# Kernel tuning notes

Hardware: AMD Instinct MI355X
Metric: run time of the kernel (lower is better)

## Reference

```python
import jax, jax.numpy as jnp
import numpy as np

BINS = 5
POINTS = 2
EPS_DIV = 1e-6
GN_GROUPS = 32
GN_EPS = 1e-5


def bilinear_sum(img, ys, xs):
    """Sum of bilinear samples with zero padding outside the image.
    img: (B, C, H, W); ys, xs: (B, K, H, W) absolute sample coords.
    Returns (B, C, H, W) = sum over K of bilinear(img, ys_k, xs_k)."""
    B, C, H, W = img.shape
    K = ys.shape[1]
    y0 = jnp.floor(ys)
    x0 = jnp.floor(xs)
    imgf = img.reshape(B, C, H * W)
    acc = jnp.zeros((B, C, K, H, W), img.dtype)
    for dy, dx in ((0, 0), (0, 1), (1, 0), (1, 1)):
        yi = y0 + dy
        xi = x0 + dx
        w = (1.0 - jnp.abs(ys - yi)) * (1.0 - jnp.abs(xs - xi))
        valid = (yi >= 0) & (yi <= H - 1) & (xi >= 0) & (xi <= W - 1)
        yc = jnp.clip(yi, 0, H - 1).astype(jnp.int32)
        xc = jnp.clip(xi, 0, W - 1).astype(jnp.int32)
        idx = (yc * W + xc).reshape(B, 1, K * H * W)
        g = jnp.take_along_axis(imgf, idx, axis=2).reshape(B, C, K, H, W)
        acc = acc + (w * valid.astype(img.dtype))[:, None] * g
    return acc.sum(axis=2)


def setup_inputs():
    key = jax.random.key(0)
    ks = jax.random.split(key, 6)
    B, C, H, W = 2, 256, 100, 152
    P, K = POINTS, BINS
    x = jax.random.normal(ks[0], (B, C, H, W), jnp.float32)
    offsets = jax.random.normal(ks[1], (B, P * K * 2, H, W), jnp.float32) * 2.0
    ef_w = jax.random.normal(ks[2], (P * C, C), jnp.float32) * 0.02
    ef_b = jnp.zeros((P * C,), jnp.float32)
    hm1_w = jax.random.normal(ks[3], (P, C, C), jnp.float32) * 0.02
    hm1_b = jnp.zeros((P, C), jnp.float32)
    hm2_w = jax.random.normal(ks[4], (P, C), jnp.float32) * 0.02
    hm2_b = jnp.zeros((P,), jnp.float32)
    merge_w = jax.random.normal(ks[5], (C, P * C), jnp.float32) * 0.02
    merge_b = jnp.zeros((C,), jnp.float32)
    gn_g = jnp.ones((C,), jnp.float32)
    gn_b = jnp.zeros((C,), jnp.float32)
    return {"x": x, "offsets": offsets, "ef_w": ef_w, "ef_b": ef_b,
            "hm1_w": hm1_w, "hm1_b": hm1_b, "hm2_w": hm2_w, "hm2_b": hm2_b,
            "merge_w": merge_w, "merge_b": merge_b, "gn_g": gn_g, "gn_b": gn_b}


def reference(x, offsets, ef_w, ef_b, hm1_w, hm1_b, hm2_w, hm2_b, merge_w, merge_b, gn_g, gn_b):
    B, C, H, W = x.shape
    P, K = POINTS, BINS
    # expand_feat: 1x1 conv C -> P*C
    ef = jnp.einsum('bchw,dc->bdhw', x, ef_w) + ef_b[None, :, None, None]
    efp = ef.reshape(B, P, C, H, W)
    # heatmap: grouped 1x1 conv (per-point) -> ReLU -> grouped 1x1 conv -> exp
    h = jax.nn.relu(jnp.einsum('bpchw,pdc->bpdhw', efp, hm1_w) + hm1_b[None, :, :, None, None])
    heat = jnp.exp(jnp.einsum('bpdhw,pd->bphw', h, hm2_w) + hm2_b[None, :, None, None])  # (B,P,H,W)
    # offsets: (B, P, K, 2, H, W) with channel layout [y, x] per bin.
    # base_offset cancels the [1,bins] kernel grid, so the deform conv with
    # all-ones weights is simply: sum over bins of bilinear samples at
    # (h + off_y, w + off_x).
    off = offsets.reshape(B, P, K, 2, H, W)
    hg = jnp.arange(H, dtype=x.dtype)[None, None, None, :, None]
    wg = jnp.arange(W, dtype=x.dtype)[None, None, None, None, :]
    ys = hg + off[:, :, :, 0]  # (B,P,K,H,W)
    xs = wg + off[:, :, :, 1]
    outs = []
    for p in range(P):
        # sample feat*heat (C channels) and heat (1 channel) together
        img = jnp.concatenate([efp[:, p] * heat[:, p][:, None], heat[:, p][:, None]], axis=1)
        s = bilinear_sum(img, ys[:, p], xs[:, p])  # (B, C+1, H, W)
        outs.append(s[:, :C] / (s[:, C:] + EPS_DIV))
    outs = jnp.concatenate(outs, axis=1)  # (B, P*C, H, W)
    merged = jnp.einsum('bchw,dc->bdhw', outs, merge_w) + merge_b[None, :, None, None]
    # GroupNorm(32, C) + ReLU
    g = merged.reshape(B, GN_GROUPS, C // GN_GROUPS, H, W)
    mu = g.mean(axis=(2, 3, 4), keepdims=True)
    var = g.var(axis=(2, 3, 4), keepdims=True)
    gn = ((g - mu) / jnp.sqrt(var + GN_EPS)).reshape(B, C, H, W)
    gn = gn * gn_g[None, :, None, None] + gn_b[None, :, None, None]
    return jax.nn.relu(gn)
```

## Files before the change

### kernel.cpp

```cpp
#include <hip/hip_runtime.h>

#define BINS 5
#define PTS  2
constexpr int Bx = 2, Cc = 256, Hh = 100, Ww = 152;
constexpr int HW = Hh * Ww;
constexpr int NTILE = 238;
constexpr float EPS_DIV = 1e-6f;
constexpr float GN_EPS  = 1e-5f;

typedef __attribute__((ext_vector_type(8))) short bfrag;
typedef __attribute__((ext_vector_type(4))) float f32x4;

__device__ __forceinline__ ushort f2bf(float f) {
    union { float f; unsigned u; } v; v.f = f;
    unsigned r = v.u + 0x7fffu + ((v.u >> 16) & 1u);
    return (ushort)(r >> 16);
}
__device__ __forceinline__ float bflo(unsigned u) {
    return __uint_as_float(u << 16);
}
__device__ __forceinline__ float bfhi(unsigned u) {
    return __uint_as_float(u & 0xffff0000u);
}
__device__ __forceinline__ unsigned pack2(float a, float b) {
    return (unsigned)f2bf(a) | ((unsigned)f2bf(b) << 16);
}

__global__ __launch_bounds__(256)
void k_wconv(const float* __restrict__ efw, const float* __restrict__ w1,
             const float* __restrict__ mw, ushort* __restrict__ wb)
{
    int gid = blockIdx.x * 256 + threadIdx.x;
    int e = gid * 4;
    int arr = e >> 17, off = e & 131071;
    const float* src = arr == 0 ? efw : (arr == 1 ? w1 : mw);
    float4 v = *(const float4*)(src + off);
    ushort4 o = { f2bf(v.x), f2bf(v.y), f2bf(v.z), f2bf(v.w) };
    *(ushort4*)(wb + e) = o;
}

__global__ __launch_bounds__(256)
void k_ef(const float* __restrict__ x, const ushort* __restrict__ wbe,
          const float* __restrict__ efb, ushort* __restrict__ efp)
{
    __shared__ ushort As[128 * 72];
    __shared__ ushort Bs[64 * 72];
    const int t = threadIdx.x;
    const int wv = t >> 6, ln = t & 63;
    const int quad = ln >> 4, l16 = ln & 15;
    const int pix0 = blockIdx.x * 64;
    const int n0 = blockIdx.y * 128;
    const int b = blockIdx.z;
    const float* xb = x + (size_t)b * Cc * HW;

    f32x4 acc[2][4];
    #pragma unroll
    for (int i = 0; i < 2; i++)
        #pragma unroll
        for (int j = 0; j < 4; j++) acc[i][j] = (f32x4){0.f, 0.f, 0.f, 0.f};

    const int arow = t >> 3, acol = (t & 7) * 8;
    const int bpix = t & 63, bkg = (t >> 6) * 8;
    int pp = pix0 + bpix; if (pp > HW - 1) pp = HW - 1;

    for (int k0 = 0; k0 < 256; k0 += 64) {
        #pragma unroll
        for (int r = 0; r < 4; r++) {
            int row = arow + r * 32;
            *(uint4*)&As[row * 72 + acol] =
                *(const uint4*)&wbe[(size_t)(n0 + row) * 256 + k0 + acol];
        }
        #pragma unroll
        for (int r = 0; r < 2; r++) {
            int kc = bkg + r * 32;
            union { ushort s[8]; uint4 v; } tmp;
            #pragma unroll
            for (int j = 0; j < 8; j++)
                tmp.s[j] = f2bf(xb[(size_t)(k0 + kc + j) * HW + pp]);
            *(uint4*)&Bs[bpix * 72 + kc] = tmp.v;
        }
        __syncthreads();
        #pragma unroll
        for (int kk = 0; kk < 64; kk += 32) {
            bfrag af[2], bfr[4];
            #pragma unroll
            for (int dt = 0; dt < 2; dt++)
                af[dt] = *(const bfrag*)&As[(wv * 32 + dt * 16 + l16) * 72 + kk + quad * 8];
            #pragma unroll
            for (int pt = 0; pt < 4; pt++)
                bfr[pt] = *(const bfrag*)&Bs[(pt * 16 + l16) * 72 + kk + quad * 8];
            #pragma unroll
            for (int dt = 0; dt < 2; dt++)
                #pragma unroll
                for (int pt = 0; pt < 4; pt++)
                    acc[dt][pt] = __builtin_amdgcn_mfma_f32_16x16x32_bf16(
                        af[dt], bfr[pt], acc[dt][pt], 0, 0, 0);
        }
        __syncthreads();
    }

    float bias[2][4];
    #pragma unroll
    for (int dt = 0; dt < 2; dt++)
        #pragma unroll
        for (int r = 0; r < 4; r++)
            bias[dt][r] = efb[n0 + wv * 32 + dt * 16 + quad * 4 + r];
    #pragma unroll
    for (int dt = 0; dt < 2; dt++)
        #pragma unroll
        for (int pt = 0; pt < 4; pt++) {
            int pix = pt * 16 + l16;
            int ch = wv * 32 + dt * 16 + quad * 4;
            ushort4 o = { f2bf(acc[dt][pt][0] + bias[dt][0]),
                          f2bf(acc[dt][pt][1] + bias[dt][1]),
                          f2bf(acc[dt][pt][2] + bias[dt][2]),
                          f2bf(acc[dt][pt][3] + bias[dt][3]) };
            *(ushort4*)&As[pix * 136 + ch] = o;
        }
    __syncthreads();
    const int p = n0 >> 8, cbase = n0 & 255;
    ushort* outb = efp + (size_t)((b * PTS + p) * HW) * Cc;
    #pragma unroll
    for (int r = 0; r < 4; r++) {
        int pix = (t >> 4) + r * 16;
        int ch8 = (t & 15) * 8;
        if (pix0 + pix < HW)
            *(uint4*)&outb[(size_t)(pix0 + pix) * Cc + cbase + ch8] =
                *(const uint4*)&As[pix * 136 + ch8];
    }
}

__global__ __launch_bounds__(256)
void k_heat(const ushort* __restrict__ efp, const ushort* __restrict__ wb1,
            const float* __restrict__ b1, const float* __restrict__ w2,
            const float* __restrict__ b2, float* __restrict__ heat)
{
    __shared__ ushort As[256 * 72];
    __shared__ ushort Bs[64 * 72];
    __shared__ float red[4][64];
    const int t = threadIdx.x;
    const int wv = t >> 6, ln = t & 63;
    const int quad = ln >> 4, l16 = ln & 15;
    const int pix0 = blockIdx.x * 64;
    const int p = blockIdx.y;
    const int b = blockIdx.z;
    const ushort* efb_ = efp + (size_t)((b * PTS + p) * HW) * Cc;
    const ushort* w1p = wb1 + (size_t)p * Cc * Cc;

    f32x4 acc[4][4];
    #pragma unroll
    for (int i = 0; i < 4; i++)
        #pragma unroll
        for (int j = 0; j < 4; j++) acc[i][j] = (f32x4){0.f, 0.f, 0.f, 0.f};

    const int srow = t >> 3, scol = (t & 7) * 8;

    for (int k0 = 0; k0 < 256; k0 += 64) {
        #pragma unroll
        for (int r = 0; r < 8; r++) {
            int row = srow + r * 32;
            *(uint4*)&As[row * 72 + scol] =
                *(const uint4*)&w1p[(size_t)row * 256 + k0 + scol];
        }
        #pragma unroll
        for (int r = 0; r < 2; r++) {
            int row = srow + r * 32;
            int pq = pix0 + row; if (pq > HW - 1) pq = HW - 1;
            *(uint4*)&Bs[row * 72 + scol] =
                *(const uint4*)&efb_[(size_t)pq * Cc + k0 + scol];
        }
        __syncthreads();
        #pragma unroll
        for (int kk = 0; kk < 64; kk += 32) {
            bfrag af[4], bfr[4];
            #pragma unroll
            for (int dt = 0; dt < 4; dt++)
                af[dt] = *(const bfrag*)&As[(wv * 64 + dt * 16 + l16) * 72 + kk + quad * 8];
            #pragma unroll
            for (int pt = 0; pt < 4; pt++)
                bfr[pt] = *(const bfrag*)&Bs[(pt * 16 + l16) * 72 + kk + quad * 8];
            #pragma unroll
            for (int dt = 0; dt < 4; dt++)
                #pragma unroll
                for (int pt = 0; pt < 4; pt++)
                    acc[dt][pt] = __builtin_amdgcn_mfma_f32_16x16x32_bf16(
                        af[dt], bfr[pt], acc[dt][pt], 0, 0, 0);
        }
        __syncthreads();
    }

    const float* b1p = b1 + p * 256;
    const float* w2p = w2 + p * 256;
    float s[4] = {0.f, 0.f, 0.f, 0.f};
    #pragma unroll
    for (int dt = 0; dt < 4; dt++) {
        int chb = wv * 64 + dt * 16 + quad * 4;
        float bb[4], ww[4];
        #pragma unroll
        for (int r = 0; r < 4; r++) { bb[r] = b1p[chb + r]; ww[r] = w2p[chb + r]; }
        #pragma unroll
        for (int pt = 0; pt < 4; pt++)
            #pragma unroll
            for (int r = 0; r < 4; r++) {
                float h = acc[dt][pt][r] + bb[r];
                h = h > 0.f ? h : 0.f;
                s[pt] += ww[r] * h;
            }
    }
    #pragma unroll
    for (int pt = 0; pt < 4; pt++) {
        s[pt] += __shfl_xor(s[pt], 16);
        s[pt] += __shfl_xor(s[pt], 32);
    }
    if (ln < 16) {
        #pragma unroll
        for (int pt = 0; pt < 4; pt++) red[wv][pt * 16 + ln] = s[pt];
    }
    __syncthreads();
    if (t < 64) {
        float v = red[0][t] + red[1][t] + red[2][t] + red[3][t] + b2[p];
        int m = pix0 + t;
        if (m < HW) heat[(size_t)(b * PTS + p) * HW + m] = expf(v);
    }
}

__global__ __launch_bounds__(256)
void k_sample(const ushort* __restrict__ efp, const float* __restrict__ heat,
              const float* __restrict__ offs, ushort* __restrict__ outs)
{
    __shared__ uint2 s_wo[32][20];
    const int t = threadIdx.x;
    const int bid = blockIdx.x;
    const int nx = (bid & 7) * 60 + (bid >> 3);
    if (nx >= 475) return;
    const int m0 = nx * 32;
    const int p = blockIdx.y;
    const int b = blockIdx.z;
    const float* heat_bp = heat + (size_t)(b * PTS + p) * HW;

    if (t < 32 * BINS) {
        int j = t / BINS, k = t % BINS;
        int hw = m0 + j;
        int hh = hw / Ww, ww = hw % Ww;
        int chy = (p * BINS + k) * 2;
        float oy = offs[((size_t)b * (PTS * BINS * 2) + chy)     * HW + hw];
        float ox = offs[((size_t)b * (PTS * BINS * 2) + chy + 1) * HW + hw];
        float ysf = (float)hh + oy;
        float xsf = (float)ww + ox;
        float y0 = floorf(ysf), x0 = floorf(xsf);
        #pragma unroll
        for (int dy = 0; dy < 2; dy++)
            #pragma unroll
            for (int dx = 0; dx < 2; dx++) {
                float yi = y0 + dy, xi = x0 + dx;
                float wgt = (1.f - fabsf(ysf - yi)) * (1.f - fabsf(xsf - xi));
                bool valid = (yi >= 0.f) && (yi <= (float)(Hh - 1)) &&
                             (xi >= 0.f) && (xi <= (float)(Ww - 1));
                int yc = (int)yi; yc = yc < 0 ? 0 : (yc > Hh - 1 ? Hh - 1 : yc);
                int xc = (int)xi; xc = xc < 0 ? 0 : (xc > Ww - 1 ? Ww - 1 : xc);
                int idx = yc * Ww + xc;
                float wh = valid ? wgt * heat_bp[idx] : 0.f;
                s_wo[j][k * 4 + dy * 2 + dx] =
                    make_uint2(__float_as_uint(wh), (unsigned)idx << 9);
            }
    }
    __syncthreads();
    if (t < 32) {
        float s = 0.f;
        #pragma unroll
        for (int u = 0; u < 20; u++) s += __uint_as_float(s_wo[t][u].x);
        float inv = 1.f / (s + EPS_DIV);
        #pragma unroll
        for (int u = 0; u < 20; u++)
            s_wo[t][u].x = __float_as_uint(__uint_as_float(s_wo[t][u].x) * inv);
    }
    __syncthreads();

    const int wv = t >> 6, ln = t & 63;
    const char* efbase = (const char*)(efp + (size_t)((b * PTS + p) * HW) * Cc)
                         + ln * 8;
    ushort* ob = outs + ((size_t)(b * HW + m0)) * (PTS * Cc) + p * Cc + ln * 4;
    #pragma unroll
    for (int i = 0; i < 8; i += 2) {
        const int j0 = wv * 8 + i, j1 = j0 + 1;
        float a0[4] = {0.f, 0.f, 0.f, 0.f};
        float a1[4] = {0.f, 0.f, 0.f, 0.f};
        #pragma unroll
        for (int u = 0; u < 20; u++) {
            uint2 wo0 = s_wo[j0][u];
            uint2 wo1 = s_wo[j1][u];
            uint2 v0 = *(const uint2*)(efbase + wo0.y);
            uint2 v1 = *(const uint2*)(efbase + wo1.y);
            float w0 = __uint_as_float(wo0.x);
            float w1 = __uint_as_float(wo1.x);
            a0[0] += w0 * bflo(v0.x); a0[1] += w0 * bfhi(v0.x);
            a0[2] += w0 * bflo(v0.y); a0[3] += w0 * bfhi(v0.y);
            a1[0] += w1 * bflo(v1.x); a1[1] += w1 * bfhi(v1.x);
            a1[2] += w1 * bflo(v1.y); a1[3] += w1 * bfhi(v1.y);
        }
        uint2 o0 = make_uint2(pack2(a0[0], a0[1]), pack2(a0[2], a0[3]));
        uint2 o1 = make_uint2(pack2(a1[0], a1[1]), pack2(a1[2], a1[3]));
        *(uint2*)(ob + (size_t)j0 * (PTS * Cc)) = o0;
        *(uint2*)(ob + (size_t)j1 * (PTS * Cc)) = o1;
    }
}

__global__ __launch_bounds__(256)
void k_merge(const ushort* __restrict__ outs, const ushort* __restrict__ wbm,
             const float* __restrict__ mb, float* __restrict__ out,
             float* __restrict__ part2)
{
    __shared__ ushort As[64 * 72];
    __shared__ ushort Bs[64 * 72];
    const int t = threadIdx.x;
    const int wv = t >> 6, ln = t & 63;
    const int quad = ln >> 4, l16 = ln & 15;
    const int pix0 = blockIdx.x * 64;
    const int n0 = blockIdx.y * 64;
    const int b = blockIdx.z;
    const ushort* ob = outs + (size_t)b * HW * (PTS * Cc);

    f32x4 acc[4];
    #pragma unroll
    for (int j = 0; j < 4; j++) acc[j] = (f32x4){0.f, 0.f, 0.f, 0.f};

    const int srow = t >> 3, scol = (t & 7) * 8;

    for (int k0 = 0; k0 < 512; k0 += 64) {
        #pragma unroll
        for (int r = 0; r < 2; r++) {
            int row = srow + r * 32;
            *(uint4*)&As[row * 72 + scol] =
                *(const uint4*)&wbm[(size_t)(n0 + row) * 512 + k0 + scol];
        }
        #pragma unroll
        for (int r = 0; r < 2; r++) {
            int row = srow + r * 32;
            int pq = pix0 + row; if (pq > HW - 1) pq = HW - 1;
            *(uint4*)&Bs[row * 72 + scol] =
                *(const uint4*)&ob[(size_t)pq * (PTS * Cc) + k0 + scol];
        }
        __syncthreads();
        #pragma unroll
        for (int kk = 0; kk < 64; kk += 32) {
            bfrag af = *(const bfrag*)&As[(wv * 16 + l16) * 72 + kk + quad * 8];
            #pragma unroll
            for (int pt = 0; pt < 4; pt++) {
                bfrag bfr = *(const bfrag*)&Bs[(pt * 16 + l16) * 72 + kk + quad * 8];
                acc[pt] = __builtin_amdgcn_mfma_f32_16x16x32_bf16(
                    af, bfr, acc[pt], 0, 0, 0);
            }
        }
        __syncthreads();
    }

    const int ch = n0 + wv * 16 + quad * 4;
    float bias[4];
    #pragma unroll
    for (int r = 0; r < 4; r++) bias[r] = mb[ch + r];

    float sacc = 0.f, qacc = 0.f;
    #pragma unroll
    for (int pt = 0; pt < 4; pt++) {
        int pix = pix0 + pt * 16 + l16;
        if (pix < HW) {
            #pragma unroll
            for (int r = 0; r < 4; r++) {
                float v = acc[pt][r] + bias[r];
                out[((size_t)b * Cc + ch + r) * HW + pix] = v;
                sacc += v; qacc += v * v;
            }
        }
    }
    #pragma unroll
    for (int off = 1; off <= 16; off <<= 1) {
        sacc += __shfl_xor(sacc, off);
        qacc += __shfl_xor(qacc, off);
    }
    if ((ln & 31) == 0) {
        int g = (n0 >> 3) + wv * 2 + (quad >> 1);
        size_t idx = ((size_t)(b * 32 + g) * NTILE + blockIdx.x) * 2;
        part2[idx + 0] = sacc;
        part2[idx + 1] = qacc;
    }
}

__global__ __launch_bounds__(256)
void k_gnfinal(const float* __restrict__ part2, float* __restrict__ statf)
{
    const int bg = blockIdx.x;
    const int t = threadIdx.x;
    float s = 0.f, q = 0.f;
    if (t < NTILE) {
        s = part2[((size_t)bg * NTILE + t) * 2 + 0];
        q = part2[((size_t)bg * NTILE + t) * 2 + 1];
    }
    #pragma unroll
    for (int off = 1; off <= 32; off <<= 1) {
        s += __shfl_xor(s, off);
        q += __shfl_xor(q, off);
    }
    __shared__ float rs[4], rq[4];
    int wid = t >> 6;
    if ((t & 63) == 0) { rs[wid] = s; rq[wid] = q; }
    __syncthreads();
    if (t == 0) {
        float S = rs[0] + rs[1] + rs[2] + rs[3];
        float Q = rq[0] + rq[1] + rq[2] + rq[3];
        const float n = 8.f * HW;
        float mean = S / n;
        float var  = Q / n - mean * mean;
        statf[bg * 2 + 0] = mean;
        statf[bg * 2 + 1] = rsqrtf(var + GN_EPS);
    }
}

__global__ __launch_bounds__(256)
void k_gnapply(float* __restrict__ out, const float* __restrict__ statf,
               const float* __restrict__ gg, const float* __restrict__ gb)
{
    const int i4 = blockIdx.x * 256 + threadIdx.x;
    const int total4 = Bx * Cc * HW / 4;
    if (i4 >= total4) return;
    const int i = i4 * 4;
    const int CHW = Cc * HW;
    const int b = i / CHW;
    const int r = i - b * CHW;
    const int c = r / HW;
    const int g = c >> 3;
    float mean = statf[(b * 32 + g) * 2 + 0];
    float istd = statf[(b * 32 + g) * 2 + 1];
    float sc = istd * gg[c];
    float sh = gb[c] - mean * sc;
    float4 v = *(float4*)(out + i);
    v.x = fmaxf(v.x * sc + sh, 0.f);
    v.y = fmaxf(v.y * sc + sh, 0.f);
    v.z = fmaxf(v.z * sc + sh, 0.f);
    v.w = fmaxf(v.w * sc + sh, 0.f);
    *(float4*)(out + i) = v;
}

extern "C" void kernel_launch(void* const* d_in, const int* in_sizes, int n_in,
                              void* d_out, int out_size, void* d_ws, size_t ws_size,
                              hipStream_t stream)
{
    const float* x    = (const float*)d_in[0];
    const float* offs = (const float*)d_in[1];
    const float* efw  = (const float*)d_in[2];
    const float* efb  = (const float*)d_in[3];
    const float* w1   = (const float*)d_in[4];
    const float* b1   = (const float*)d_in[5];
    const float* w2   = (const float*)d_in[6];
    const float* b2   = (const float*)d_in[7];
    const float* mw   = (const float*)d_in[8];
    const float* mb   = (const float*)d_in[9];
    const float* gg   = (const float*)d_in[10];
    const float* gb   = (const float*)d_in[11];
    float* out = (float*)d_out;

    ushort* wb    = (ushort*)d_ws;
    ushort* wbe   = wb;
    ushort* wb1   = wb + 131072;
    ushort* wbm   = wb + 262144;
    ushort* efp   = wb + 393216;
    ushort* outsb = efp + (size_t)Bx * PTS * HW * Cc;
    float*  heat  = (float*)(outsb + (size_t)Bx * HW * PTS * Cc);
    float*  part2 = heat + (size_t)Bx * PTS * HW;
    float*  statf = part2 + (size_t)64 * NTILE * 2;

    dim3 blk(256);
    k_wconv  <<<dim3(384),              blk, 0, stream>>>(efw, w1, mw, wb);
    k_ef     <<<dim3(238, 4, Bx),       blk, 0, stream>>>(x, wbe, efb, efp);
    k_heat   <<<dim3(238, PTS, Bx),     blk, 0, stream>>>(efp, wb1, b1, w2, b2, heat);
    k_sample <<<dim3(480, PTS, Bx),     blk, 0, stream>>>(efp, heat, offs, outsb);
    k_merge  <<<dim3(NTILE, 4, Bx),     blk, 0, stream>>>(outsb, wbm, mb, out, part2);
    k_gnfinal<<<dim3(64),               blk, 0, stream>>>(part2, statf);
    k_gnapply<<<dim3(Bx * Cc * HW / 4 / 256), blk, 0, stream>>>(out, statf, gg, gb);
}
```

Measured before the change: 214.3 us.

## Pre-transpose input to bf16, widen sample loads, store merge output as bf16

Adds a transpose kernel that converts x to pixel-major bf16, so the expand GEMM can load its B tile with vectorized 16-byte reads instead of strided scalar fp32 loads. The sampling loop now has each lane gather 8 channels with one 16-byte load rather than two 4-channel loads. The merge GEMM writes a bf16 intermediate that the GroupNorm apply pass reads and expands into the fp32 output, cutting intermediate traffic. These add an extra launch and a workspace buffer, and put one more bf16 rounding on the pre-norm values.

```diff
diff --git a/kernel.cpp b/kernel.cpp
--- a/kernel.cpp
+++ b/kernel.cpp
@@ -40,7 +40,29 @@
 }
 
 __global__ __launch_bounds__(256)
-void k_ef(const float* __restrict__ x, const ushort* __restrict__ wbe,
+void k_xt(const float* __restrict__ x, ushort* __restrict__ xbt)
+{
+    __shared__ float tile[32][33];
+    const int t = threadIdx.x;
+    const int hw0 = blockIdx.x * 32;
+    const int c0 = blockIdx.y * 32;
+    const int b = blockIdx.z;
+    const float* xb = x + ((size_t)b * Cc + c0) * HW + hw0;
+    const int tx = t & 31, ty = t >> 5;
+    #pragma unroll
+    for (int r = 0; r < 4; r++) {
+        int c = ty + r * 8;
+        tile[c][tx] = xb[(size_t)c * HW + tx];
+    }
+    __syncthreads();
+    const int hwl = t >> 3, c4 = (t & 7) * 4;
+    ushort4 o = { f2bf(tile[c4 + 0][hwl]), f2bf(tile[c4 + 1][hwl]),
+                  f2bf(tile[c4 + 2][hwl]), f2bf(tile[c4 + 3][hwl]) };
+    *(ushort4*)&xbt[((size_t)b * HW + hw0 + hwl) * Cc + c0 + c4] = o;
+}
+
+__global__ __launch_bounds__(256)
+void k_ef(const ushort* __restrict__ xbt, const ushort* __restrict__ wbe,
           const float* __restrict__ efb, ushort* __restrict__ efp)
 {
     __shared__ ushort As[128 * 72];
@@ -51,7 +73,7 @@
     const int pix0 = blockIdx.x * 64;
     const int n0 = blockIdx.y * 128;
     const int b = blockIdx.z;
-    const float* xb = x + (size_t)b * Cc * HW;
+    const ushort* xb = xbt + (size_t)b * HW * Cc;
 
     f32x4 acc[2][4];
     #pragma unroll
@@ -60,8 +82,7 @@
         for (int j = 0; j < 4; j++) acc[i][j] = (f32x4){0.f, 0.f, 0.f, 0.f};
 
     const int arow = t >> 3, acol = (t & 7) * 8;
-    const int bpix = t & 63, bkg = (t >> 6) * 8;
-    int pp = pix0 + bpix; if (pp > HW - 1) pp = HW - 1;
+    const int srow = t >> 3, scol = (t & 7) * 8;
 
     for (int k0 = 0; k0 < 256; k0 += 64) {
         #pragma unroll
@@ -72,12 +93,10 @@
         }
         #pragma unroll
         for (int r = 0; r < 2; r++) {
-            int kc = bkg + r * 32;
-            union { ushort s[8]; uint4 v; } tmp;
-            #pragma unroll
-            for (int j = 0; j < 8; j++)
-                tmp.s[j] = f2bf(xb[(size_t)(k0 + kc + j) * HW + pp]);
-            *(uint4*)&Bs[bpix * 72 + kc] = tmp.v;
+            int row = srow + r * 32;
+            int pq = pix0 + row; if (pq > HW - 1) pq = HW - 1;
+            *(uint4*)&Bs[row * 72 + scol] =
+                *(const uint4*)&xb[(size_t)pq * Cc + k0 + scol];
         }
         __syncthreads();
         #pragma unroll
@@ -277,37 +296,33 @@
     __syncthreads();
 
     const int wv = t >> 6, ln = t & 63;
+    const int half = ln >> 5, c8 = ln & 31;
     const char* efbase = (const char*)(efp + (size_t)((b * PTS + p) * HW) * Cc)
-                         + ln * 8;
-    ushort* ob = outs + ((size_t)(b * HW + m0)) * (PTS * Cc) + p * Cc + ln * 4;
+                         + c8 * 16;
+    ushort* ob = outs + ((size_t)(b * HW + m0)) * (PTS * Cc) + p * Cc + c8 * 8;
     #pragma unroll
     for (int i = 0; i < 8; i += 2) {
-        const int j0 = wv * 8 + i, j1 = j0 + 1;
-        float a0[4] = {0.f, 0.f, 0.f, 0.f};
-        float a1[4] = {0.f, 0.f, 0.f, 0.f};
+        const int j = wv * 8 + i + half;
+        float a[8] = {0.f, 0.f, 0.f, 0.f, 0.f, 0.f, 0.f, 0.f};
         #pragma unroll
         for (int u = 0; u < 20; u++) {
-            uint2 wo0 = s_wo[j0][u];
-            uint2 wo1 = s_wo[j1][u];
-            uint2 v0 = *(const uint2*)(efbase + wo0.y);
-            uint2 v1 = *(const uint2*)(efbase + wo1.y);
-            float w0 = __uint_as_float(wo0.x);
-            float w1 = __uint_as_float(wo1.x);
-            a0[0] += w0 * bflo(v0.x); a0[1] += w0 * bfhi(v0.x);
-            a0[2] += w0 * bflo(v0.y); a0[3] += w0 * bfhi(v0.y);
-            a1[0] += w1 * bflo(v1.x); a1[1] += w1 * bfhi(v1.x);
-            a1[2] += w1 * bflo(v1.y); a1[3] += w1 * bfhi(v1.y);
-        }
-        uint2 o0 = make_uint2(pack2(a0[0], a0[1]), pack2(a0[2], a0[3]));
-        uint2 o1 = make_uint2(pack2(a1[0], a1[1]), pack2(a1[2], a1[3]));
-        *(uint2*)(ob + (size_t)j0 * (PTS * Cc)) = o0;
-        *(uint2*)(ob + (size_t)j1 * (PTS * Cc)) = o1;
+            uint2 wo = s_wo[j][u];
+            uint4 v = *(const uint4*)(efbase + wo.y);
+            float w = __uint_as_float(wo.x);
+            a[0] += w * bflo(v.x); a[1] += w * bfhi(v.x);
+            a[2] += w * bflo(v.y); a[3] += w * bfhi(v.y);
+            a[4] += w * bflo(v.z); a[5] += w * bfhi(v.z);
+            a[6] += w * bflo(v.w); a[7] += w * bfhi(v.w);
+        }
+        uint4 o = { pack2(a[0], a[1]), pack2(a[2], a[3]),
+                    pack2(a[4], a[5]), pack2(a[6], a[7]) };
+        *(uint4*)(ob + (size_t)j * (PTS * Cc)) = o;
     }
 }
 
 __global__ __launch_bounds__(256)
 void k_merge(const ushort* __restrict__ outs, const ushort* __restrict__ wbm,
-             const float* __restrict__ mb, float* __restrict__ out,
+             const float* __restrict__ mb, ushort* __restrict__ mgb,
              float* __restrict__ part2)
 {
     __shared__ ushort As[64 * 72];
@@ -367,7 +382,7 @@
             #pragma unroll
             for (int r = 0; r < 4; r++) {
                 float v = acc[pt][r] + bias[r];
-                out[((size_t)b * Cc + ch + r) * HW + pix] = v;
+                mgb[((size_t)b * Cc + ch + r) * HW + pix] = f2bf(v);
                 sacc += v; qacc += v * v;
             }
         }
@@ -416,13 +431,12 @@
 }
 
 __global__ __launch_bounds__(256)
-void k_gnapply(float* __restrict__ out, const float* __restrict__ statf,
-               const float* __restrict__ gg, const float* __restrict__ gb)
-{
-    const int i4 = blockIdx.x * 256 + threadIdx.x;
-    const int total4 = Bx * Cc * HW / 4;
-    if (i4 >= total4) return;
-    const int i = i4 * 4;
+void k_gnapply(const ushort* __restrict__ mgb, const float* __restrict__ statf,
+               const float* __restrict__ gg, const float* __restrict__ gb,
+               float* __restrict__ out)
+{
+    const int i8 = blockIdx.x * 256 + threadIdx.x;
+    const int i = i8 * 8;
     const int CHW = Cc * HW;
     const int b = i / CHW;
     const int r = i - b * CHW;
@@ -432,12 +446,18 @@
     float istd = statf[(b * 32 + g) * 2 + 1];
     float sc = istd * gg[c];
     float sh = gb[c] - mean * sc;
-    float4 v = *(float4*)(out + i);
-    v.x = fmaxf(v.x * sc + sh, 0.f);
-    v.y = fmaxf(v.y * sc + sh, 0.f);
-    v.z = fmaxf(v.z * sc + sh, 0.f);
-    v.w = fmaxf(v.w * sc + sh, 0.f);
-    *(float4*)(out + i) = v;
+    uint4 v = *(const uint4*)(mgb + i);
+    float4 o0, o1;
+    o0.x = fmaxf(bflo(v.x) * sc + sh, 0.f);
+    o0.y = fmaxf(bfhi(v.x) * sc + sh, 0.f);
+    o0.z = fmaxf(bflo(v.y) * sc + sh, 0.f);
+    o0.w = fmaxf(bfhi(v.y) * sc + sh, 0.f);
+    o1.x = fmaxf(bflo(v.z) * sc + sh, 0.f);
+    o1.y = fmaxf(bfhi(v.z) * sc + sh, 0.f);
+    o1.z = fmaxf(bflo(v.w) * sc + sh, 0.f);
+    o1.w = fmaxf(bfhi(v.w) * sc + sh, 0.f);
+    *(float4*)(out + i)     = o0;
+    *(float4*)(out + i + 4) = o1;
 }
 
 extern "C" void kernel_launch(void* const* d_in, const int* in_sizes, int n_in,
@@ -464,16 +484,19 @@
     ushort* wbm   = wb + 262144;
     ushort* efp   = wb + 393216;
     ushort* outsb = efp + (size_t)Bx * PTS * HW * Cc;
-    float*  heat  = (float*)(outsb + (size_t)Bx * HW * PTS * Cc);
+    ushort* xbt   = outsb + (size_t)Bx * HW * PTS * Cc;
+    ushort* mgb   = xbt + (size_t)Bx * HW * Cc;
+    float*  heat  = (float*)(mgb + (size_t)Bx * Cc * HW);
     float*  part2 = heat + (size_t)Bx * PTS * HW;
     float*  statf = part2 + (size_t)64 * NTILE * 2;
 
     dim3 blk(256);
     k_wconv  <<<dim3(384),              blk, 0, stream>>>(efw, w1, mw, wb);
-    k_ef     <<<dim3(238, 4, Bx),       blk, 0, stream>>>(x, wbe, efb, efp);
+    k_xt     <<<dim3(475, 8, Bx),       blk, 0, stream>>>(x, xbt);
+    k_ef     <<<dim3(238, 4, Bx),       blk, 0, stream>>>(xbt, wbe, efb, efp);
     k_heat   <<<dim3(238, PTS, Bx),     blk, 0, stream>>>(efp, wb1, b1, w2, b2, heat);
     k_sample <<<dim3(480, PTS, Bx),     blk, 0, stream>>>(efp, heat, offs, outsb);
-    k_merge  <<<dim3(NTILE, 4, Bx),     blk, 0, stream>>>(outsb, wbm, mb, out, part2);
+    k_merge  <<<dim3(NTILE, 4, Bx),     blk, 0, stream>>>(outsb, wbm, mb, mgb, part2);
     k_gnfinal<<<dim3(64),               blk, 0, stream>>>(part2, statf);
-    k_gnapply<<<dim3(Bx * Cc * HW / 4 / 256), blk, 0, stream>>>(out, statf, gg, gb);
-}
+    k_gnapply<<<dim3(Bx * Cc * HW / 8 / 256), blk, 0, stream>>>(mgb, statf, gg, gb, out);
+}
```

After: 212.3 us. Within noise of the previous version (-1.0%).
